# Performance work log

Measured on AMD Instinct MI355X. Metric: run time of the kernel, lower is better.

## Reference

```python
import jax, jax.numpy as jnp
import numpy as np

B, NX, NY, F = 4, 4096, 4096, 16

def setup_inputs() -> dict:
    key = jax.random.key(0)
    k1, k2, k3, k4, k5 = jax.random.split(key, 5)
    return {
        "x": jax.random.normal(k1, (B, NX, 3), dtype=jnp.float32),
        "y": jax.random.normal(k2, (B, NY, 3), dtype=jnp.float32),
        "sample_x": jax.random.uniform(k3, (B, NX, F), dtype=jnp.float32),
        "sample_y": jax.random.uniform(k4, (B, NY, F), dtype=jnp.float32),
        "scale": jax.random.uniform(k5, (F,), dtype=jnp.float32),
    }

def reference(x, y, sample_x, sample_y, scale):
    sq_x = jnp.sum(x * x, axis=-1, keepdims=True)            # (B,NX,1)
    sq_y = jnp.sum(y * y, axis=-1, keepdims=True)            # (B,NY,1)
    dot = jnp.einsum('bnd,bmd->bnm', x, y)                   # (B,NX,NY)
    d = jnp.clip(sq_x + jnp.swapaxes(sq_y, -2, -1) - 2.0 * dot, 1e-10, 1e6)
    # fixed-scale branch
    s = jnp.clip(scale, 1e-6, 1e6)
    scale_x = jnp.clip(jnp.einsum('bnf,f->bn', sample_x, s), 1e-10, 1e6)  # (B,NX)
    scale_y = jnp.clip(jnp.einsum('bmf,f->bm', sample_y, s), 1e-10, 1e6)  # (B,NY)
    scale_xy = jnp.sqrt(jnp.clip(scale_x[:, :, None] * scale_y[:, None, :], 1e-10, 1e12))
    return 1.0 / (1.0 + d / scale_xy)
```

## Files before the change

### kernel.cpp

```cpp
#include <hip/hip_runtime.h>


constexpr int kB  = 4;
constexpr int kNX = 4096;
constexpr int kNY = 4096;
constexpr int kF  = 16;

__global__ __launch_bounds__(256) void row_stats_kernel(
    const float* __restrict__ x, const float* __restrict__ y,
    const float* __restrict__ sx, const float* __restrict__ sy,
    const float* __restrict__ scale,
    float2* __restrict__ rx, float2* __restrict__ ry, int nper)
{
    int t = blockIdx.x * blockDim.x + threadIdx.x;
    if (t >= 2 * nper) return;
    const float* pts; const float* smp; float2* dst; int idx;
    if (t < nper) { pts = x; smp = sx; dst = rx; idx = t; }
    else          { pts = y; smp = sy; dst = ry; idx = t - nper; }

    const float* p = pts + (size_t)idx * 3;
    float sq = p[0] * p[0] + p[1] * p[1] + p[2] * p[2];

    const float4* s4 = (const float4*)(smp + (size_t)idx * kF);
    const float4* c4 = (const float4*)scale;
    float acc = 0.f;
#pragma unroll
    for (int k = 0; k < kF / 4; ++k) {
        float4 sv = s4[k];
        float4 cv = c4[k];
        acc += sv.x * fminf(fmaxf(cv.x, 1e-6f), 1e6f);
        acc += sv.y * fminf(fmaxf(cv.y, 1e-6f), 1e6f);
        acc += sv.z * fminf(fmaxf(cv.z, 1e-6f), 1e6f);
        acc += sv.w * fminf(fmaxf(cv.w, 1e-6f), 1e6f);
    }
    float sc = fminf(fmaxf(acc, 1e-10f), 1e6f);
    dst[idx] = make_float2(sq, __builtin_amdgcn_sqrtf(sc));
}

__global__ __launch_bounds__(256) void cauchy_main_kernel(
    const float* __restrict__ x, const float* __restrict__ y,
    const float2* __restrict__ rx, const float2* __restrict__ ry,
    float* __restrict__ out)
{
    const int hw   = blockIdx.x;
    const int jc   = ((hw & 3) << 8) | threadIdx.x;
    const int j0   = jc << 2;
    const int qrow = hw >> 2;

#pragma unroll 1
    for (int bb = 0; bb < kB; ++bb) {
        const float4* yv = (const float4*)(y + ((size_t)bb * kNY + j0) * 3);
        float4 ya = yv[0], yb = yv[1], yc = yv[2];
        const float4* ryv = (const float4*)(ry + (size_t)bb * kNY + j0);
        float4 r01 = ryv[0], r23 = ryv[1];

        const float yxx[4] = {ya.x, ya.w, yb.z, yc.y};
        const float yyy[4] = {ya.y, yb.x, yb.w, yc.z};
        const float yzz[4] = {ya.z, yb.y, yc.x, yc.w};
        const float sqy[4] = {r01.x, r01.z, r23.x, r23.z};
        const float scy[4] = {r01.y, r01.w, r23.y, r23.w};

#pragma unroll
        for (int h = 0; h < 2; ++h) {
            const int i0 = ((h << 9) | qrow) << 2;

            const float4* xv = (const float4*)(x + ((size_t)bb * kNX + i0) * 3);
            float4 xa = xv[0], xb = xv[1], xc = xv[2];
            const float4* rxv = (const float4*)(rx + (size_t)bb * kNX + i0);
            float4 q01 = rxv[0], q23 = rxv[1];

            const float xxx[4] = {xa.x, xa.w, xb.z, xc.y};
            const float xyy[4] = {xa.y, xb.x, xb.w, xc.z};
            const float xzz[4] = {xa.z, xb.y, xc.x, xc.w};
            const float sqx[4] = {q01.x, q01.z, q23.x, q23.z};
            const float scx[4] = {q01.y, q01.w, q23.y, q23.w};

            size_t obase = ((size_t)bb * kNX + i0) * (size_t)kNY + j0;
#pragma unroll
            for (int r = 0; r < 4; ++r) {
                float4 o;
                float* op = (float*)&o;
#pragma unroll
                for (int k = 0; k < 4; ++k) {
                    float dot = xxx[r] * yxx[k] + xyy[r] * yyy[k] + xzz[r] * yzz[k];
                    float d = fmaf(-2.f, dot, sqx[r] + sqy[k]);
                    d = fminf(fmaxf(d, 1e-10f), 1e6f);
                    float s = fmaxf(scx[r] * scy[k], 1e-5f);
                    op[k] = s * __builtin_amdgcn_rcpf(s + d);
                }
                *(float4*)(out + obase + (size_t)r * kNY) = o;
            }
        }
    }
}

__global__ __launch_bounds__(256) void cauchy_fallback_kernel(
    const float* __restrict__ x, const float* __restrict__ y,
    const float* __restrict__ sx, const float* __restrict__ sy,
    const float* __restrict__ scale, float* __restrict__ out)
{
    const int t = blockIdx.x * 256 + threadIdx.x;
    const int jc = t & (kNY / 4 - 1);
    const int rowtile = t >> 10;
    const int b  = rowtile >> 10;
    const int i0 = (rowtile & (kNX / 4 - 1)) << 2;
    const int j0 = jc << 2;

    float4 c[4];
    const float4* c4 = (const float4*)scale;
#pragma unroll
    for (int k = 0; k < 4; ++k) {
        float4 cv = c4[k];
        c[k].x = fminf(fmaxf(cv.x, 1e-6f), 1e6f);
        c[k].y = fminf(fmaxf(cv.y, 1e-6f), 1e6f);
        c[k].z = fminf(fmaxf(cv.z, 1e-6f), 1e6f);
        c[k].w = fminf(fmaxf(cv.w, 1e-6f), 1e6f);
    }

    const float4* yv = (const float4*)(y + ((size_t)b * kNY + j0) * 3);
    float4 ya = yv[0], yb = yv[1], yc = yv[2];
    const float4* xv = (const float4*)(x + ((size_t)b * kNX + i0) * 3);
    float4 xa = xv[0], xb = xv[1], xc = xv[2];

    const float yxx[4] = {ya.x, ya.w, yb.z, yc.y};
    const float yyy[4] = {ya.y, yb.x, yb.w, yc.z};
    const float yzz[4] = {ya.z, yb.y, yc.x, yc.w};
    const float xxx[4] = {xa.x, xa.w, xb.z, xc.y};
    const float xyy[4] = {xa.y, xb.x, xb.w, xc.z};
    const float xzz[4] = {xa.z, xb.y, xc.x, xc.w};

    float sqx[4], scx[4], sqy[4], scy[4];
#pragma unroll
    for (int r = 0; r < 4; ++r) {
        sqx[r] = xxx[r] * xxx[r] + xyy[r] * xyy[r] + xzz[r] * xzz[r];
        sqy[r] = yxx[r] * yxx[r] + yyy[r] * yyy[r] + yzz[r] * yzz[r];
        const float4* a4 = (const float4*)(sx + ((size_t)b * kNX + i0 + r) * kF);
        const float4* b4 = (const float4*)(sy + ((size_t)b * kNY + j0 + r) * kF);
        float accx = 0.f, accy = 0.f;
#pragma unroll
        for (int k = 0; k < 4; ++k) {
            float4 av = a4[k], bv = b4[k], cv = c[k];
            accx += av.x * cv.x + av.y * cv.y + av.z * cv.z + av.w * cv.w;
            accy += bv.x * cv.x + bv.y * cv.y + bv.z * cv.z + bv.w * cv.w;
        }
        scx[r] = __builtin_amdgcn_sqrtf(fminf(fmaxf(accx, 1e-10f), 1e6f));
        scy[r] = __builtin_amdgcn_sqrtf(fminf(fmaxf(accy, 1e-10f), 1e6f));
    }

    size_t obase = ((size_t)b * kNX + i0) * (size_t)kNY + j0;
#pragma unroll
    for (int r = 0; r < 4; ++r) {
        float4 o;
        float* op = (float*)&o;
#pragma unroll
        for (int k = 0; k < 4; ++k) {
            float dot = xxx[r] * yxx[k] + xyy[r] * yyy[k] + xzz[r] * yzz[k];
            float d = fmaf(-2.f, dot, sqx[r] + sqy[k]);
            d = fminf(fmaxf(d, 1e-10f), 1e6f);
            float s = fmaxf(scx[r] * scy[k], 1e-5f);
            op[k] = s * __builtin_amdgcn_rcpf(s + d);
        }
        *(float4*)(out + obase + (size_t)r * kNY) = o;
    }
}

extern "C" void kernel_launch(void* const* d_in, const int* in_sizes, int n_in,
                              void* d_out, int out_size, void* d_ws, size_t ws_size,
                              hipStream_t stream) {
    const float* x     = (const float*)d_in[0];
    const float* y     = (const float*)d_in[1];
    const float* sx    = (const float*)d_in[2];
    const float* sy    = (const float*)d_in[3];
    const float* scale = (const float*)d_in[4];
    float* out = (float*)d_out;

    const int nper = kB * kNX;
    const size_t need = (size_t)2 * nper * sizeof(float2);

    if (ws_size >= need) {
        float2* rx = (float2*)d_ws;
        float2* ry = rx + nper;
        row_stats_kernel<<<(2 * nper + 255) / 256, 256, 0, stream>>>(
            x, y, sx, sy, scale, rx, ry, nper);
        cauchy_main_kernel<<<2048, 256, 0, stream>>>(x, y, rx, ry, out);
    } else {
        const int fb_blocks = (kB * kNX * kNY / 16) / 256;
        cauchy_fallback_kernel<<<fb_blocks, 256, 0, stream>>>(
            x, y, sx, sy, scale, out);
    }
}
```

Baseline: 263.0 us.

## Restructure main kernel to per-row stripes with y cached in registers

Each block now handles 16 consecutive full rows of one batch. Every thread keeps four column groups of y coordinates and stats in registers and streams x one row at a time. This is meant to produce long contiguous output row writes and to reuse the y loads across more rows, replacing the earlier scattered row-tile pattern that looped over batches. It raises register pressure, halves the block count, and adds a launch-bounds occupancy hint.

Result: no change. 267.3 us (+1.6%).

```diff
diff --git a/kernel.cpp b/kernel.cpp
--- a/kernel.cpp
+++ b/kernel.cpp
@@ -5,6 +5,8 @@
 constexpr int kNX = 4096;
 constexpr int kNY = 4096;
 constexpr int kF  = 16;
+constexpr int kRowsPerBlk = 16;
+constexpr int kMainBlks = kB * kNX / kRowsPerBlk;
 
 __global__ __launch_bounds__(256) void row_stats_kernel(
     const float* __restrict__ x, const float* __restrict__ y,
@@ -37,59 +39,54 @@
     dst[idx] = make_float2(sq, __builtin_amdgcn_sqrtf(sc));
 }
 
-__global__ __launch_bounds__(256) void cauchy_main_kernel(
+__global__ __launch_bounds__(256, 2) void cauchy_main_kernel(
     const float* __restrict__ x, const float* __restrict__ y,
     const float2* __restrict__ rx, const float2* __restrict__ ry,
     float* __restrict__ out)
 {
-    const int hw   = blockIdx.x;
-    const int jc   = ((hw & 3) << 8) | threadIdx.x;
-    const int j0   = jc << 2;
-    const int qrow = hw >> 2;
+    const int blk  = blockIdx.x;
+    const int b    = blk >> 8;
+    const int row0 = (blk & 255) * kRowsPerBlk;
+    const int t    = threadIdx.x;
 
-#pragma unroll 1
-    for (int bb = 0; bb < kB; ++bb) {
-        const float4* yv = (const float4*)(y + ((size_t)bb * kNY + j0) * 3);
+    float yxx[4][4], yyy[4][4], yzz[4][4], sqy[4][4], scy[4][4];
+#pragma unroll
+    for (int s = 0; s < 4; ++s) {
+        const int j0 = ((s << 8) | t) << 2;
+        const float4* yv = (const float4*)(y + ((size_t)b * kNY + j0) * 3);
         float4 ya = yv[0], yb = yv[1], yc = yv[2];
-        const float4* ryv = (const float4*)(ry + (size_t)bb * kNY + j0);
+        const float4* ryv = (const float4*)(ry + (size_t)b * kNY + j0);
         float4 r01 = ryv[0], r23 = ryv[1];
+        yxx[s][0] = ya.x; yxx[s][1] = ya.w; yxx[s][2] = yb.z; yxx[s][3] = yc.y;
+        yyy[s][0] = ya.y; yyy[s][1] = yb.x; yyy[s][2] = yb.w; yyy[s][3] = yc.z;
+        yzz[s][0] = ya.z; yzz[s][1] = yb.y; yzz[s][2] = yc.x; yzz[s][3] = yc.w;
+        sqy[s][0] = r01.x; sqy[s][1] = r01.z; sqy[s][2] = r23.x; sqy[s][3] = r23.z;
+        scy[s][0] = r01.y; scy[s][1] = r01.w; scy[s][2] = r23.y; scy[s][3] = r23.w;
+    }
 
-        const float yxx[4] = {ya.x, ya.w, yb.z, yc.y};
-        const float yyy[4] = {ya.y, yb.x, yb.w, yc.z};
-        const float yzz[4] = {ya.z, yb.y, yc.x, yc.w};
-        const float sqy[4] = {r01.x, r01.z, r23.x, r23.z};
-        const float scy[4] = {r01.y, r01.w, r23.y, r23.w};
+#pragma unroll 2
+    for (int r = 0; r < kRowsPerBlk; ++r) {
+        const int i = row0 + r;
+        const float* xp = x + ((size_t)b * kNX + i) * 3;
+        const float xx = xp[0], xy = xp[1], xz = xp[2];
+        const float2 st = rx[(size_t)b * kNX + i];
+        const float sqx = st.x, scx = st.y;
 
+        const size_t rowbase = ((size_t)b * kNX + i) * (size_t)kNY;
 #pragma unroll
-        for (int h = 0; h < 2; ++h) {
-            const int i0 = ((h << 9) | qrow) << 2;
-
-            const float4* xv = (const float4*)(x + ((size_t)bb * kNX + i0) * 3);
-            float4 xa = xv[0], xb = xv[1], xc = xv[2];
-            const float4* rxv = (const float4*)(rx + (size_t)bb * kNX + i0);
-            float4 q01 = rxv[0], q23 = rxv[1];
-
-            const float xxx[4] = {xa.x, xa.w, xb.z, xc.y};
-            const float xyy[4] = {xa.y, xb.x, xb.w, xc.z};
-            const float xzz[4] = {xa.z, xb.y, xc.x, xc.w};
-            const float sqx[4] = {q01.x, q01.z, q23.x, q23.z};
-            const float scx[4] = {q01.y, q01.w, q23.y, q23.w};
-
-            size_t obase = ((size_t)bb * kNX + i0) * (size_t)kNY + j0;
+        for (int s = 0; s < 4; ++s) {
+            const int j0 = ((s << 8) | t) << 2;
+            float4 o;
+            float* op = (float*)&o;
 #pragma unroll
-            for (int r = 0; r < 4; ++r) {
-                float4 o;
-                float* op = (float*)&o;
-#pragma unroll
-                for (int k = 0; k < 4; ++k) {
-                    float dot = xxx[r] * yxx[k] + xyy[r] * yyy[k] + xzz[r] * yzz[k];
-                    float d = fmaf(-2.f, dot, sqx[r] + sqy[k]);
-                    d = fminf(fmaxf(d, 1e-10f), 1e6f);
-                    float s = fmaxf(scx[r] * scy[k], 1e-5f);
-                    op[k] = s * __builtin_amdgcn_rcpf(s + d);
-                }
-                *(float4*)(out + obase + (size_t)r * kNY) = o;
+            for (int k = 0; k < 4; ++k) {
+                float dot = xx * yxx[s][k] + xy * yyy[s][k] + xz * yzz[s][k];
+                float d = fmaf(-2.f, dot, sqx + sqy[s][k]);
+                d = fminf(fmaxf(d, 1e-10f), 1e6f);
+                float sc = fmaxf(scx * scy[s][k], 1e-5f);
+                op[k] = sc * __builtin_amdgcn_rcpf(sc + d);
             }
+            *(float4*)(out + rowbase + j0) = o;
         }
     }
 }
@@ -182,7 +179,7 @@
         float2* ry = rx + nper;
         row_stats_kernel<<<(2 * nper + 255) / 256, 256, 0, stream>>>(
             x, y, sx, sy, scale, rx, ry, nper);
-        cauchy_main_kernel<<<2048, 256, 0, stream>>>(x, y, rx, ry, out);
+        cauchy_main_kernel<<<kMainBlks, 256, 0, stream>>>(x, y, rx, ry, out);
     } else {
         const int fb_blocks = (kB * kNX * kNY / 16) / 256;
         cauchy_fallback_kernel<<<fb_blocks, 256, 0, stream>>>(
```
